# Kernel tuning notes

Hardware: AMD Instinct MI355X
Metric: run time of the kernel (lower is better)

## Reference

```python
import jax, jax.numpy as jnp
import numpy as np

B, T, E, H, A = 64, 1024, 512, 512, 512  # batch, src_len, enc_dim, hidden, attention_dim
D_IN = 512                                # decoder input embedding dim; cell input = D_IN + E


def setup_inputs() -> dict:
    key = jax.random.key(0)
    ks = jax.random.split(key, 10)
    s = 0.05  # small init to keep tanh/sigmoid unsaturated
    return {
        "inputs":  jax.random.normal(ks[0], (B, D_IN), jnp.float32),
        "states":  jax.random.normal(ks[1], (B, H), jnp.float32),
        "encoded": jax.random.normal(ks[2], (B, T, E), jnp.float32),
        "W_enc":   jax.random.normal(ks[3], (E, A), jnp.float32) * s,
        "W_state": jax.random.normal(ks[4], (H, A), jnp.float32) * s,
        "v":       jax.random.normal(ks[5], (A,), jnp.float32) * s,
        "W_ih":    jax.random.normal(ks[6], (3 * H, D_IN + E), jnp.float32) * s,
        "W_hh":    jax.random.normal(ks[7], (3 * H, H), jnp.float32) * s,
        "b_ih":    jnp.zeros((3 * H,), jnp.float32),
        "b_hh":    jnp.zeros((3 * H,), jnp.float32),
    }


def reference(inputs, states, encoded, W_enc, W_state, v, W_ih, W_hh, b_ih, b_hh):
    # --- Bahdanau additive attention (one decoder step) ---
    enc_proj = jnp.einsum("bte,ea->bta", encoded, W_enc)      # setup_memory projection
    st_proj = states @ W_state                                  # [B,A]
    scores = jnp.tanh(enc_proj + st_proj[:, None, :]) @ v       # [B,T]
    weights = jax.nn.softmax(scores, axis=-1)                   # [B,T]
    context = jnp.einsum("bt,bte->be", weights, encoded)       # [B,E]

    # --- GRU cell step on concat(inputs, context) (torch.nn.GRUCell math) ---
    x = jnp.concatenate([inputs, context], axis=-1)             # [B, D_IN+E]
    gi = x @ W_ih.T + b_ih                                      # [B, 3H]
    gh = states @ W_hh.T + b_hh                                 # [B, 3H]
    i_r, i_z, i_n = jnp.split(gi, 3, axis=-1)
    h_r, h_z, h_n = jnp.split(gh, 3, axis=-1)
    r = jax.nn.sigmoid(i_r + h_r)
    z = jax.nn.sigmoid(i_z + h_z)
    n = jnp.tanh(i_n + r * h_n)
    return (1.0 - z) * n + z * states                           # [B,H]
```

## Files before the change

### kernel.cpp

```cpp
#include <hip/hip_runtime.h>
#include <hip/hip_bf16.h>

#define BN   64
#define TN   1024
#define EN   512
#define AN   512
#define HN   512
#define G3H  1536

typedef __bf16 bf16x8 __attribute__((ext_vector_type(8)));
typedef __bf16 bf16x4 __attribute__((ext_vector_type(4)));
typedef float  f32x8  __attribute__((ext_vector_type(8)));
typedef float  f32x4  __attribute__((ext_vector_type(4)));
typedef unsigned int uint4v __attribute__((ext_vector_type(4)));

__device__ __forceinline__ float fast_tanh(float x) {
    float e = __expf(2.0f * x);
    return 1.0f - 2.0f / (e + 1.0f);
}
__device__ __forceinline__ float fast_sigmoid(float x) {
    return 1.0f / (1.0f + __expf(-x));
}

#define GL2LDS16(gsrc, ldst)                                                  \
    __builtin_amdgcn_global_load_lds(                                         \
        (const __attribute__((address_space(1))) unsigned int*)(gsrc),        \
        (__attribute__((address_space(3))) unsigned int*)(ldst), 16, 0, 0)

__global__ __launch_bounds__(256) void prep_kernel(
    const float* __restrict__ states, const float* __restrict__ W_enc,
    const float* __restrict__ W_state, const float* __restrict__ inputs,
    const float* __restrict__ W_ih, const float* __restrict__ W_hh,
    float* __restrict__ stp, __bf16* __restrict__ wencT,
    __bf16* __restrict__ xbf, __bf16* __restrict__ stbf,
    __bf16* __restrict__ wihbf, __bf16* __restrict__ whhbf,
    float* __restrict__ scores)
{
    __shared__ float srow[512];
    int blk = blockIdx.x, tid = threadIdx.x;

    if (blk < 64) {
        int b = blk;
        srow[tid] = states[b * 512 + tid];
        srow[tid + 256] = states[b * 512 + tid + 256];
        __syncthreads();
        int n0 = tid, n1 = tid + 256;
        float a0 = 0.f, a1 = 0.f;
        for (int k = 0; k < 512; ++k) {
            float s = srow[k];
            a0 += s * W_state[k * 512 + n0];
            a1 += s * W_state[k * 512 + n1];
        }
        stp[b * 512 + n0] = a0;
        stp[b * 512 + n1] = a1;
    } else if (blk < 72) {
        int n = (blk - 64) * 64 + (tid & 63);
        int cseg = tid >> 6;
        for (int c = cseg * 16; c < cseg * 16 + 16; ++c) {
            f32x8 f;
            #pragma unroll
            for (int j = 0; j < 8; ++j) f[j] = W_enc[(c * 8 + j) * 512 + n];
            int cs = (c & ~7) | ((c & 7) ^ (n & 7));
            *(bf16x8*)(wencT + n * 512 + cs * 8) = __builtin_convertvector(f, bf16x8);
        }
    } else if (blk < 840) {
        int base4 = (blk - 72) * 512 + tid * 2;
        #pragma unroll
        for (int j = 0; j < 2; ++j) {
            int i4 = base4 + j;
            f32x4 f = *(const f32x4*)(W_ih + i4 * 4);
            *(bf16x4*)(wihbf + i4 * 4) = __builtin_convertvector(f, bf16x4);
        }
    } else if (blk < 1224) {
        int base4 = (blk - 840) * 512 + tid * 2;
        #pragma unroll
        for (int j = 0; j < 2; ++j) {
            int i4 = base4 + j;
            f32x4 f = *(const f32x4*)(W_hh + i4 * 4);
            *(bf16x4*)(whhbf + i4 * 4) = __builtin_convertvector(f, bf16x4);
        }
    } else if (blk < 1240) {
        int base4 = (blk - 1224) * 512 + tid * 2;
        #pragma unroll
        for (int j = 0; j < 2; ++j) {
            int i4 = base4 + j;
            int e = i4 * 4;
            int b = e >> 9, c = e & 511;
            f32x4 f = *(const f32x4*)(inputs + e);
            *(bf16x4*)(xbf + b * 1024 + c) = __builtin_convertvector(f, bf16x4);
        }
    } else if (blk < 1256) {
        int base4 = (blk - 1240) * 512 + tid * 2;
        #pragma unroll
        for (int j = 0; j < 2; ++j) {
            int i4 = base4 + j;
            int e = i4 * 4;
            f32x4 f = *(const f32x4*)(states + e);
            *(bf16x4*)(stbf + e) = __builtin_convertvector(f, bf16x4);
        }
    } else {
        int e = (blk - 1256) * 1024 + tid * 4;
        *(f32x4*)(scores + e) = (f32x4){0.f, 0.f, 0.f, 0.f};
    }
}

__global__ __launch_bounds__(256, 3) void score_kernel(
    const float* __restrict__ enc, const __bf16* __restrict__ wencT,
    const float* __restrict__ stp, const float* __restrict__ v,
    float* __restrict__ scores)
{
    __shared__ __align__(16) __bf16 As[128 * 64];
    __shared__ __align__(16) __bf16 Bs[128 * 64];
    __shared__ float sacc[256];

    int tid = threadIdx.x;
    int bid = blockIdx.x;
    int orig = (bid & 7) * 256 + (bid >> 3);
    int rt = orig >> 2, ct = orig & 3;
    int grow0 = rt * 128;
    int c0 = ct * 128;
    int b = grow0 >> 10;

    int lane = tid & 63, wid = tid >> 6;
    int wrow = wid >> 1, wcol = wid & 1;
    int l15 = lane & 15, g = lane >> 4;

    f32x4 acc[4][4];
    #pragma unroll
    for (int m = 0; m < 4; ++m)
        #pragma unroll
        for (int n = 0; n < 4; ++n) acc[m][n] = (f32x4){0.f, 0.f, 0.f, 0.f};

    for (int ks = 0; ks < 8; ++ks) {
        #pragma unroll
        for (int i = 0; i < 4; ++i) {
            int p = i * 256 + tid;
            int row = p >> 3, c = p & 7;
            const __bf16* src = wencT + (size_t)(c0 + row) * 512 + ks * 64 + c * 8;
            char* dst = (char*)Bs + (i * 256 + wid * 64) * 16;
            GL2LDS16(src, dst);
        }
        #pragma unroll
        for (int i = 0; i < 4; ++i) {
            int p = i * 256 + tid;
            int row = p >> 3, c = p & 7;
            f32x8 f = *(const f32x8*)(enc + (size_t)(grow0 + row) * 512 + ks * 64 + c * 8);
            int cs = c ^ (row & 7);
            *(bf16x8*)((char*)As + row * 128 + cs * 16) = __builtin_convertvector(f, bf16x8);
        }
        __syncthreads();
        #pragma unroll
        for (int kk = 0; kk < 2; ++kk) {
            bf16x8 af[4], bfr[4];
            #pragma unroll
            for (int m = 0; m < 4; ++m) {
                int row = wrow * 64 + m * 16 + l15;
                int cch = (kk * 4 + g) ^ (row & 7);
                af[m] = *(const bf16x8*)((char*)As + row * 128 + cch * 16);
            }
            #pragma unroll
            for (int n = 0; n < 4; ++n) {
                int row = wcol * 64 + n * 16 + l15;
                int cch = (kk * 4 + g) ^ (row & 7);
                bfr[n] = *(const bf16x8*)((char*)Bs + row * 128 + cch * 16);
            }
            #pragma unroll
            for (int m = 0; m < 4; ++m)
                #pragma unroll
                for (int n = 0; n < 4; ++n)
                    acc[m][n] = __builtin_amdgcn_mfma_f32_16x16x32_bf16(
                        af[m], bfr[n], acc[m][n], 0, 0, 0);
        }
        if (ks < 7) __syncthreads();
    }

    float sv[4], vw[4];
    #pragma unroll
    for (int n = 0; n < 4; ++n) {
        int col = c0 + wcol * 64 + n * 16 + l15;
        sv[n] = stp[b * 512 + col];
        vw[n] = v[col];
    }
    float rp[16];
    #pragma unroll
    for (int i = 0; i < 16; ++i) rp[i] = 0.f;
    #pragma unroll
    for (int m = 0; m < 4; ++m)
        #pragma unroll
        for (int n = 0; n < 4; ++n) {
            #pragma unroll
            for (int r = 0; r < 4; ++r)
                rp[m * 4 + r] += vw[n] * fast_tanh(acc[m][n][r] + sv[n]);
        }
    #pragma unroll
    for (int i = 0; i < 16; ++i) {
        rp[i] += __shfl_xor(rp[i], 1);
        rp[i] += __shfl_xor(rp[i], 2);
        rp[i] += __shfl_xor(rp[i], 4);
        rp[i] += __shfl_xor(rp[i], 8);
    }
    if (l15 == 0) {
        #pragma unroll
        for (int m = 0; m < 4; ++m)
            #pragma unroll
            for (int r = 0; r < 4; ++r)
                sacc[wcol * 128 + wrow * 64 + m * 16 + g * 4 + r] = rp[m * 4 + r];
    }
    __syncthreads();
    if (tid < 128)
        atomicAdd(scores + grow0 + tid, sacc[tid] + sacc[128 + tid]);
}

__global__ __launch_bounds__(256) void ctx_kernel(
    const float* __restrict__ scores, const float* __restrict__ enc,
    __bf16* __restrict__ xbf)
{
    __shared__ float wsm[1024];
    __shared__ float red[512];
    __shared__ float tmp[8];
    int tid = threadIdx.x, lane = tid & 63, w = tid >> 6;
    int b = blockIdx.x >> 2, c0 = (blockIdx.x & 3) * 128;

    f32x4 s = *(const f32x4*)(scores + b * 1024 + tid * 4);
    float m = fmaxf(fmaxf(s[0], s[1]), fmaxf(s[2], s[3]));
    #pragma unroll
    for (int off = 32; off >= 1; off >>= 1) m = fmaxf(m, __shfl_xor(m, off));
    if (lane == 0) tmp[w] = m;
    __syncthreads();
    float M = fmaxf(fmaxf(tmp[0], tmp[1]), fmaxf(tmp[2], tmp[3]));
    float e0 = __expf(s[0] - M), e1 = __expf(s[1] - M);
    float e2 = __expf(s[2] - M), e3 = __expf(s[3] - M);
    wsm[tid * 4 + 0] = e0; wsm[tid * 4 + 1] = e1;
    wsm[tid * 4 + 2] = e2; wsm[tid * 4 + 3] = e3;
    float sum = e0 + e1 + e2 + e3;
    #pragma unroll
    for (int off = 32; off >= 1; off >>= 1) sum += __shfl_xor(sum, off);
    if (lane == 0) tmp[4 + w] = sum;
    __syncthreads();
    float S = tmp[4] + tmp[5] + tmp[6] + tmp[7];

    const float* ep = enc + ((b * 1024 + w * 256) * 512 + c0 + lane * 2);
    float ax = 0.f, ay = 0.f;
    #pragma unroll 4
    for (int t = 0; t < 256; ++t) {
        float wt = wsm[w * 256 + t];
        float2 ev = *(const float2*)(ep + t * 512);
        ax += wt * ev.x;
        ay += wt * ev.y;
    }
    red[w * 128 + lane * 2] = ax;
    red[w * 128 + lane * 2 + 1] = ay;
    __syncthreads();
    if (tid < 128) {
        float c = (red[tid] + red[128 + tid] + red[256 + tid] + red[384 + tid]) / S;
        xbf[b * 1024 + 512 + c0 + tid] = (__bf16)c;
    }
}

__global__ __launch_bounds__(256) void gru_gemm(
    const __bf16* __restrict__ xbf, const __bf16* __restrict__ stbf,
    const __bf16* __restrict__ wihbf, const __bf16* __restrict__ whhbf,
    const float* __restrict__ b_ih, const float* __restrict__ b_hh,
    float* __restrict__ gi, float* __restrict__ gh)
{
    __shared__ __align__(16) __bf16 As[64 * 72];
    __shared__ __align__(16) __bf16 Bs[128 * 72];
    int blk = blockIdx.x, tid = threadIdx.x;
    bool is_gh = blk >= 12;
    int n0 = (is_gh ? blk - 12 : blk) * 128;
    int K = is_gh ? 512 : 1024;
    const __bf16* Aptr = is_gh ? stbf : xbf;
    const __bf16* Bptr = is_gh ? whhbf : wihbf;
    const float* bias = is_gh ? b_hh : b_ih;
    float* outp = is_gh ? gh : gi;

    int lane = tid & 63, wid = tid >> 6, l15 = lane & 15, g = lane >> 4;
    f32x4 acc[4][2];
    #pragma unroll
    for (int i = 0; i < 4; ++i)
        #pragma unroll
        for (int j = 0; j < 2; ++j) acc[i][j] = (f32x4){0.f, 0.f, 0.f, 0.f};

    int nkc = K >> 6;
    for (int kc = 0; kc < nkc; ++kc) {
        int k0 = kc * 64;
        #pragma unroll
        for (int q = 0; q < 2; ++q) {
            int ch = tid * 2 + q, row = ch >> 3, seg = ch & 7;
            uint4v u = *(const uint4v*)(Aptr + row * K + k0 + seg * 8);
            *(uint4v*)(As + row * 72 + seg * 8) = u;
        }
        #pragma unroll
        for (int q = 0; q < 4; ++q) {
            int ch = tid * 4 + q, row = ch >> 3, seg = ch & 7;
            uint4v u = *(const uint4v*)(Bptr + (n0 + row) * K + k0 + seg * 8);
            *(uint4v*)(Bs + row * 72 + seg * 8) = u;
        }
        __syncthreads();
        #pragma unroll
        for (int kk = 0; kk < 2; ++kk) {
            bf16x8 af[4], bfr[2];
            #pragma unroll
            for (int m = 0; m < 4; ++m)
                af[m] = *(const bf16x8*)(As + (m * 16 + l15) * 72 + kk * 32 + g * 8);
            #pragma unroll
            for (int n = 0; n < 2; ++n)
                bfr[n] = *(const bf16x8*)(Bs + (wid * 32 + n * 16 + l15) * 72 + kk * 32 + g * 8);
            #pragma unroll
            for (int m = 0; m < 4; ++m)
                #pragma unroll
                for (int n = 0; n < 2; ++n)
                    acc[m][n] = __builtin_amdgcn_mfma_f32_16x16x32_bf16(
                        af[m], bfr[n], acc[m][n], 0, 0, 0);
        }
        __syncthreads();
    }
    #pragma unroll
    for (int m = 0; m < 4; ++m)
        #pragma unroll
        for (int n = 0; n < 2; ++n) {
            int col = n0 + wid * 32 + n * 16 + l15;
            float bb = bias[col];
            #pragma unroll
            for (int r = 0; r < 4; ++r) {
                int brow = m * 16 + g * 4 + r;
                outp[brow * 1536 + col] = acc[m][n][r] + bb;
            }
        }
}

__global__ __launch_bounds__(256) void gru_gates(
    const float* __restrict__ gi, const float* __restrict__ gh,
    const float* __restrict__ states, float* __restrict__ out)
{
    int i = blockIdx.x * 256 + threadIdx.x;
    int b = i >> 9, j = i & 511;
    const float* gib = gi + b * 1536;
    const float* ghb = gh + b * 1536;
    float r = fast_sigmoid(gib[j] + ghb[j]);
    float z = fast_sigmoid(gib[512 + j] + ghb[512 + j]);
    float n = fast_tanh(gib[1024 + j] + r * ghb[1024 + j]);
    out[i] = (1.f - z) * n + z * states[i];
}

extern "C" void kernel_launch(void* const* d_in, const int* in_sizes, int n_in,
                              void* d_out, int out_size, void* d_ws, size_t ws_size,
                              hipStream_t stream)
{
    const float* inputs  = (const float*)d_in[0];
    const float* states  = (const float*)d_in[1];
    const float* encoded = (const float*)d_in[2];
    const float* W_enc   = (const float*)d_in[3];
    const float* W_state = (const float*)d_in[4];
    const float* v       = (const float*)d_in[5];
    const float* W_ih    = (const float*)d_in[6];
    const float* W_hh    = (const float*)d_in[7];
    const float* b_ih    = (const float*)d_in[8];
    const float* b_hh    = (const float*)d_in[9];
    float* out = (float*)d_out;
    char* ws = (char*)d_ws;

    float*  stp    = (float*)(ws + 0);
    __bf16* wencT  = (__bf16*)(ws + 131072);
    float*  scores = (float*)(ws + 655360);
    __bf16* xbf    = (__bf16*)(ws + 917504);
    __bf16* stbf   = (__bf16*)(ws + 1048576);
    __bf16* wihbf  = (__bf16*)(ws + 1114112);
    __bf16* whhbf  = (__bf16*)(ws + 4259840);
    float*  gi     = (float*)(ws + 5832704);
    float*  gh     = (float*)(ws + 6225920);

    prep_kernel<<<1320, 256, 0, stream>>>(states, W_enc, W_state, inputs, W_ih, W_hh,
                                          stp, wencT, xbf, stbf, wihbf, whhbf, scores);
    score_kernel<<<2048, 256, 0, stream>>>(encoded, wencT, stp, v, scores);
    ctx_kernel<<<256, 256, 0, stream>>>(scores, encoded, xbf);
    gru_gemm<<<24, 256, 0, stream>>>(xbf, stbf, wihbf, whhbf, b_ih, b_hh, gi, gh);
    gru_gates<<<128, 256, 0, stream>>>(gi, gh, states, out);
}
```

Baseline: 126.3 us.

## Software-pipeline score GEMM with register-prefetched A and double-buffered B

Restructures the score kernel K-loop so the fp32 encoder tile for step ks+2 is loaded into registers and the bf16 weight tile is DMA'd into an alternate LDS buffer while the current step's MFMAs run. Explicit vmcnt waits and raw barriers replace __syncthreads to control how far ahead loads can run, and s_setprio raises wave priority around the MFMA block. This is meant to hide global-load latency behind compute, at the cost of extra LDS and registers (more pressure at 3 blocks per SM) and hand-tuned waitcnt values that must match the issued load count.

```diff
diff --git a/kernel.cpp b/kernel.cpp
--- a/kernel.cpp
+++ b/kernel.cpp
@@ -110,7 +110,7 @@
     float* __restrict__ scores)
 {
     __shared__ __align__(16) __bf16 As[128 * 64];
-    __shared__ __align__(16) __bf16 Bs[128 * 64];
+    __shared__ __align__(16) __bf16 Bs[2][128 * 64];
     __shared__ float sacc[256];
 
     int tid = threadIdx.x;
@@ -131,24 +131,49 @@
         #pragma unroll
         for (int n = 0; n < 4; ++n) acc[m][n] = (f32x4){0.f, 0.f, 0.f, 0.f};
 
-    for (int ks = 0; ks < 8; ++ks) {
+    f32x8 aReg[4];
+
+    auto load_A = [&](int ks) {
+        #pragma unroll
+        for (int i = 0; i < 4; ++i) {
+            int p = i * 256 + tid;
+            int row = p >> 3, c = p & 7;
+            aReg[i] = *(const f32x8*)(enc + (size_t)(grow0 + row) * 512 + ks * 64 + c * 8);
+        }
+    };
+    auto write_A = [&]() {
+        #pragma unroll
+        for (int i = 0; i < 4; ++i) {
+            int p = i * 256 + tid;
+            int row = p >> 3, c = p & 7;
+            int cs = c ^ (row & 7);
+            *(bf16x8*)((char*)As + row * 128 + cs * 16) =
+                __builtin_convertvector(aReg[i], bf16x8);
+        }
+    };
+    auto stage_B = [&](int ks, int buf) {
         #pragma unroll
         for (int i = 0; i < 4; ++i) {
             int p = i * 256 + tid;
             int row = p >> 3, c = p & 7;
             const __bf16* src = wencT + (size_t)(c0 + row) * 512 + ks * 64 + c * 8;
-            char* dst = (char*)Bs + (i * 256 + wid * 64) * 16;
+            char* dst = (char*)Bs[buf] + (i * 256 + wid * 64) * 16;
             GL2LDS16(src, dst);
         }
-        #pragma unroll
-        for (int i = 0; i < 4; ++i) {
-            int p = i * 256 + tid;
-            int row = p >> 3, c = p & 7;
-            f32x8 f = *(const f32x8*)(enc + (size_t)(grow0 + row) * 512 + ks * 64 + c * 8);
-            int cs = c ^ (row & 7);
-            *(bf16x8*)((char*)As + row * 128 + cs * 16) = __builtin_convertvector(f, bf16x8);
-        }
-        __syncthreads();
+    };
+
+    load_A(0);
+    stage_B(0, 0);
+    write_A();
+    load_A(1);
+    stage_B(1, 1);
+    asm volatile("s_waitcnt vmcnt(12) lgkmcnt(0)" ::: "memory");
+    __builtin_amdgcn_s_barrier();
+    __builtin_amdgcn_sched_barrier(0);
+
+    #pragma unroll
+    for (int ks = 0; ks < 8; ++ks) {
+        const char* Bcur = (const char*)Bs[ks & 1];
         #pragma unroll
         for (int kk = 0; kk < 2; ++kk) {
             bf16x8 af[4], bfr[4];
@@ -162,16 +187,31 @@
             for (int n = 0; n < 4; ++n) {
                 int row = wcol * 64 + n * 16 + l15;
                 int cch = (kk * 4 + g) ^ (row & 7);
-                bfr[n] = *(const bf16x8*)((char*)Bs + row * 128 + cch * 16);
+                bfr[n] = *(const bf16x8*)(Bcur + row * 128 + cch * 16);
             }
+            __builtin_amdgcn_s_setprio(1);
             #pragma unroll
             for (int m = 0; m < 4; ++m)
                 #pragma unroll
                 for (int n = 0; n < 4; ++n)
                     acc[m][n] = __builtin_amdgcn_mfma_f32_16x16x32_bf16(
                         af[m], bfr[n], acc[m][n], 0, 0, 0);
-        }
-        if (ks < 7) __syncthreads();
+            __builtin_amdgcn_s_setprio(0);
+        }
+        if (ks < 7) {
+            __builtin_amdgcn_s_barrier();
+            __builtin_amdgcn_sched_barrier(0);
+            write_A();
+            if (ks < 6) {
+                load_A(ks + 2);
+                stage_B(ks + 2, ks & 1);
+                asm volatile("s_waitcnt vmcnt(12) lgkmcnt(0)" ::: "memory");
+            } else {
+                asm volatile("s_waitcnt vmcnt(0) lgkmcnt(0)" ::: "memory");
+            }
+            __builtin_amdgcn_s_barrier();
+            __builtin_amdgcn_sched_barrier(0);
+        }
     }
 
     float sv[4], vw[4];
@@ -199,6 +239,7 @@
         rp[i] += __shfl_xor(rp[i], 4);
         rp[i] += __shfl_xor(rp[i], 8);
     }
+    __syncthreads();
     if (l15 == 0) {
         #pragma unroll
         for (int m = 0; m < 4; ++m)
```

Result: slower. 134.2 us (+6.2%).
